# Optimization experiments

Hardware: AMD Instinct MI355X
Metric: run time of the kernel (lower is better)

Reference implementation:

```python
import jax, jax.numpy as jnp
import numpy as np

N_NODES = 50000
N_EDGES = 800000
DIM = 128
N_LAYERS = 3
OUT_DIM = 2
W_SCALE = 0.02


def setup_inputs() -> dict:
    key = jax.random.key(0)
    ks = jax.random.split(key, 12)
    x = jax.random.normal(ks[0], (N_NODES, DIM), dtype=jnp.float32)
    src = jax.random.randint(ks[1], (N_EDGES,), 0, N_NODES, dtype=jnp.int32)
    dst = jax.random.randint(ks[2], (N_EDGES,), 0, N_NODES, dtype=jnp.int32)
    Vw = jax.random.normal(ks[3], (N_LAYERS, DIM, DIM), dtype=jnp.float32) * W_SCALE
    Vb = jax.random.normal(ks[4], (N_LAYERS, DIM), dtype=jnp.float32) * W_SCALE
    Aw = jax.random.normal(ks[5], (N_LAYERS, DIM, DIM), dtype=jnp.float32) * W_SCALE
    Ab = jax.random.normal(ks[6], (N_LAYERS, DIM), dtype=jnp.float32) * W_SCALE
    Rw = jax.random.normal(ks[7], (N_LAYERS, DIM, DIM), dtype=jnp.float32) * W_SCALE
    Rb = jax.random.normal(ks[8], (N_LAYERS, DIM), dtype=jnp.float32) * W_SCALE
    out_w = jax.random.normal(ks[9], (OUT_DIM, DIM), dtype=jnp.float32) * W_SCALE
    out_b = jax.random.normal(ks[10], (OUT_DIM,), dtype=jnp.float32) * W_SCALE
    return {"x": x, "src": src, "dst": dst, "Vw": Vw, "Vb": Vb, "Aw": Aw,
            "Ab": Ab, "Rw": Rw, "Rb": Rb, "out_w": out_w, "out_b": out_b}


def reference(x, src, dst, Vw, Vb, Aw, Ab, Rw, Rb, out_w, out_b):
    # x: [N, d]; src/dst: [E] (edge (dst_i <- src_i): out[dst] += h[src], as torch.spmm(Adj, h))
    N = x.shape[0]
    h = x
    for l in range(Vw.shape[0]):
        # sum aggregation over neighbors; learn_eps=False adds self-loops -> + h
        agg = jax.ops.segment_sum(h[src], dst, num_segments=N) + h  # [N, d]
        ro = jnp.sum(h, axis=0, keepdims=True)                      # sum readout, [1, d]
        # trainable combine: relu(V(h) + A(agg) + R(readout)), R term broadcasts over nodes
        h = jax.nn.relu(h @ Vw[l].T + Vb[l]
                        + agg @ Aw[l].T + Ab[l]
                        + ro @ Rw[l].T + Rb[l])
    # node task, recursive_weighting=False: sigmoid(Linear(h))
    return jax.nn.sigmoid(h @ out_w.T + out_b)
```

## Files before the change

### kernel.cpp

```cpp
#include <hip/hip_runtime.h>
#include <cstdint>
#include <cstddef>

#define NN 50000
#define NE 800000
#define D 128
#define KK 256
#define NPAD 50048
#define GEMM_BLOCKS (NPAD / 64)
#define LDSW 136
#define BSTR 136
#define NBUCK 196
#define BCAP 5120
#define SCH 4096
#define SBLKS ((NE + SCH - 1) / SCH)
#define CVT_BLOCKS 391
#define PREP_BLOCKS 384
#define AGG_BLOCKS 12500

typedef __bf16 bf16x8 __attribute__((ext_vector_type(8)));
typedef float f32x4 __attribute__((ext_vector_type(4)));
typedef float f32x2 __attribute__((ext_vector_type(2)));
typedef unsigned short ushort;
typedef unsigned int uint;

__device__ __forceinline__ ushort f2b(float f) {
    uint u = __float_as_uint(f);
    uint r = (u + 0x7fffu + ((u >> 16) & 1u)) >> 16;
    return (ushort)r;
}
__device__ __forceinline__ float blo(uint u) { return __uint_as_float(u << 16); }
__device__ __forceinline__ float bhi(uint u) { return __uint_as_float(u & 0xffff0000u); }

__device__ __forceinline__ uint enc_n(float v) {
    int t = (int)(__float_as_uint(v) >> 22);
    int n = max(t - 252, min(t - 251, 1));
    return (uint)min(max(n, 0), 7);
}
__device__ __forceinline__ uint enc8(uint4 vv, float sf) {
    uint n0 = enc_n(blo(vv.x) * sf), n1 = enc_n(bhi(vv.x) * sf);
    uint n2 = enc_n(blo(vv.y) * sf), n3 = enc_n(bhi(vv.y) * sf);
    uint n4 = enc_n(blo(vv.z) * sf), n5 = enc_n(bhi(vv.z) * sf);
    uint n6 = enc_n(blo(vv.w) * sf), n7 = enc_n(bhi(vv.w) * sf);
    return n0 | (n1 << 4) | (n2 << 8) | (n3 << 12) |
           (n4 << 16) | (n5 << 20) | (n6 << 24) | (n7 << 28);
}
__device__ __forceinline__ void dec_acc(uint u, float* a) {
    uint lo = u & 0x0F0F0F0Fu;
    uint hi = (u >> 4) & 0x0F0F0F0Fu;
    uint b0 = __builtin_amdgcn_perm(0x4C484440u, 0x3C383000u, lo);
    uint b1 = __builtin_amdgcn_perm(0x4C484440u, 0x3C383000u, hi);
    f32x2 p;
    p = __builtin_amdgcn_cvt_pk_f32_fp8(b0, false); a[0] += p.x; a[2] += p.y;
    p = __builtin_amdgcn_cvt_pk_f32_fp8(b0, true);  a[4] += p.x; a[6] += p.y;
    p = __builtin_amdgcn_cvt_pk_f32_fp8(b1, false); a[1] += p.x; a[3] += p.y;
    p = __builtin_amdgcn_cvt_pk_f32_fp8(b1, true);  a[5] += p.x; a[7] += p.y;
}

__device__ __forceinline__ void red_col(const float* __restrict__ pblk, int nb,
                                        int j, float* __restrict__ dst,
                                        float* __restrict__ sred) {
    int t = threadIdx.x;
    float s = 0.f;
    for (int b = t; b < nb; b += 256) s += pblk[(size_t)b * D + j];
#pragma unroll
    for (int off = 32; off; off >>= 1) s += __shfl_xor(s, off);
    if ((t & 63) == 0) sred[t >> 6] = s;
    __syncthreads();
    if (t == 0) dst[j] = sred[0] + sred[1] + sred[2] + sred[3];
}

__global__ void k_zero(int* __restrict__ zone) { zone[threadIdx.x] = 0; }

__global__ void __launch_bounds__(256) k_build(
    const int* __restrict__ src, const int* __restrict__ dst,
    int* __restrict__ bfill, uint* __restrict__ packed,
    const float* __restrict__ x, ushort* __restrict__ hb,
    uint* __restrict__ hf4, float* __restrict__ pblk,
    const float* __restrict__ Vw, const float* __restrict__ Aw,
    ushort* __restrict__ W2) {
    __shared__ int cnt[256];
    __shared__ int base[256];
    __shared__ ushort pos[SCH];
    __shared__ float scol[D];
    int t = threadIdx.x;
    if (blockIdx.x < SBLKS) {
        int e0 = blockIdx.x * SCH, e1 = min(e0 + SCH, NE);
        cnt[t] = 0;
        __syncthreads();
        for (int e = e0 + t; e < e1; e += 256) {
            int b = dst[e] >> 8;
            pos[e - e0] = (ushort)atomicAdd(&cnt[b], 1);
        }
        __syncthreads();
        if (t < NBUCK && cnt[t])
            base[t] = atomicAdd(&bfill[t], cnt[t]) + t * BCAP;
        __syncthreads();
        for (int e = e0 + t; e < e1; e += 256) {
            int d = dst[e];
            int b = d >> 8;
            packed[base[b] + pos[e - e0]] = (uint)src[e] | ((uint)(d & 255) << 16);
        }
        return;
    }
    if (blockIdx.x < SBLKS + CVT_BLOCKS) {
        int bid = blockIdx.x - SBLKS;
        if (t < D) scol[t] = 0.f;
        __syncthreads();
        const float4* x4 = (const float4*)x;
        uint4* h8 = (uint4*)hb;
        float cs[8] = {0, 0, 0, 0, 0, 0, 0, 0};
        int bb = bid * 2048 + t;
#pragma unroll
        for (int i = 0; i < 8; i++) {
            int idx = bb + i * 256;
            if (idx < NN * D / 8) {
                float4 va = x4[idx * 2], vb = x4[idx * 2 + 1];
                cs[0] += va.x; cs[1] += va.y; cs[2] += va.z; cs[3] += va.w;
                cs[4] += vb.x; cs[5] += vb.y; cs[6] += vb.z; cs[7] += vb.w;
                uint4 o;
                o.x = (uint)f2b(va.x) | ((uint)f2b(va.y) << 16);
                o.y = (uint)f2b(va.z) | ((uint)f2b(va.w) << 16);
                o.z = (uint)f2b(vb.x) | ((uint)f2b(vb.y) << 16);
                o.w = (uint)f2b(vb.z) | ((uint)f2b(vb.w) << 16);
                h8[idx] = o;
                uint n0 = enc_n(fmaxf(va.x * 0.75f + 3.f, 0.f));
                uint n1 = enc_n(fmaxf(va.y * 0.75f + 3.f, 0.f));
                uint n2 = enc_n(fmaxf(va.z * 0.75f + 3.f, 0.f));
                uint n3 = enc_n(fmaxf(va.w * 0.75f + 3.f, 0.f));
                uint n4 = enc_n(fmaxf(vb.x * 0.75f + 3.f, 0.f));
                uint n5 = enc_n(fmaxf(vb.y * 0.75f + 3.f, 0.f));
                uint n6 = enc_n(fmaxf(vb.z * 0.75f + 3.f, 0.f));
                uint n7 = enc_n(fmaxf(vb.w * 0.75f + 3.f, 0.f));
                hf4[idx] = n0 | (n1 << 4) | (n2 << 8) | (n3 << 12) |
                           (n4 << 16) | (n5 << 20) | (n6 << 24) | (n7 << 28);
            }
        }
#pragma unroll
        for (int k = 0; k < 8; k++) {
            cs[k] += __shfl_xor(cs[k], 16);
            cs[k] += __shfl_xor(cs[k], 32);
        }
        if ((t & 63) < 16) {
            int c8 = (t & 15) * 8;
#pragma unroll
            for (int k = 0; k < 8; k++) atomicAdd(&scol[c8 + k], cs[k]);
        }
        __syncthreads();
        if (t < D) pblk[(size_t)bid * D + t] = scol[t];
        return;
    }
    int idx = (blockIdx.x - SBLKS - CVT_BLOCKS) * 256 + t;
    int k = idx & (KK - 1);
    int j = (idx >> 8) & (D - 1);
    int l = idx >> 15;
    float v = (k < D) ? Vw[((size_t)l * D + j) * D + k]
                      : Aw[((size_t)l * D + j) * D + (k - D)];
    W2[idx] = f2b(v);
}

__global__ void __launch_bounds__(512) k_bcsr(
    const uint* __restrict__ packed, const int* __restrict__ bfill,
    int* __restrict__ esrc, int2* __restrict__ rp2,
    const float* __restrict__ pblk, float* __restrict__ ro0) {
    __shared__ int hist[256];
    __shared__ int sc[256];
    __shared__ int start[256];
    __shared__ ushort pos[BCAP];
    __shared__ float sred[8];
    int t = threadIdx.x;
    if (blockIdx.x >= NBUCK) {
        int j = blockIdx.x - NBUCK;
        if (t < 256) {
            float s = 0.f;
            for (int b = t; b < CVT_BLOCKS; b += 256) s += pblk[(size_t)b * D + j];
#pragma unroll
            for (int off = 32; off; off >>= 1) s += __shfl_xor(s, off);
            if ((t & 63) == 0) sred[t >> 6] = s;
        }
        __syncthreads();
        if (t == 0) ro0[j] = sred[0] + sred[1] + sred[2] + sred[3];
        return;
    }
    int b = blockIdx.x;
    int lo = b * BCAP, cnt = bfill[b];
    if (t < 256) hist[t] = 0;
    __syncthreads();
    for (int i = t; i < cnt; i += 512) {
        int node = (packed[lo + i] >> 16) & 255;
        pos[i] = (ushort)atomicAdd(&hist[node], 1);
    }
    __syncthreads();
    int v = 0;
    if (t < 256) { v = hist[t]; sc[t] = v; }
    __syncthreads();
    for (int off = 1; off < 256; off <<= 1) {
        int u = 0;
        if (t < 256 && t >= off) u = sc[t - off];
        __syncthreads();
        if (t < 256) sc[t] += u;
        __syncthreads();
    }
    if (t < 256) {
        int excl = sc[t] - v;
        int node = b * 256 + t;
        if (node < NN) rp2[node] = make_int2(lo + excl, lo + excl + v);
        start[t] = lo + excl;
    }
    __syncthreads();
    for (int i = t; i < cnt; i += 512) {
        uint p = packed[lo + i];
        esrc[start[(p >> 16) & 255] + pos[i]] = (int)(p & 0xffffu);
    }
}

__global__ void __launch_bounds__(256) k_agg(
    const ushort* __restrict__ hb, const uint* __restrict__ hf4,
    const int2* __restrict__ rp2, const int* __restrict__ esrc,
    const float* __restrict__ slot, ushort* __restrict__ A1, int lay0,
    const float* __restrict__ pblk, float* __restrict__ ro_out) {
    if (blockIdx.x >= AGG_BLOCKS) {
        __shared__ float sred[8];
        int j = blockIdx.x - AGG_BLOCKS;
        red_col(pblk, GEMM_BLOCKS, j, ro_out, sred);
        return;
    }
    int wave = (blockIdx.x * blockDim.x + threadIdx.x) >> 6;
    int lane = threadIdx.x & 63;
    if (wave >= NN) return;
    int c = lane & 15, s = lane >> 4;
    float dsc = lay0 ? (4.f / 3.f) : fmaxf(slot[0], 0.5f) * (1.f / 3.f);
    float doff = lay0 ? 4.f : 0.f;
    float a[8] = {0, 0, 0, 0, 0, 0, 0, 0};
    int2 rp = rp2[wave];
    int e0 = rp.x, e1 = rp.y;
    int cnt = e1 - e0;
    int iters = (cnt + 3) >> 2;
    int i0 = e0 + s;
    for (int it = 0; it < iters; it += 4) {
        int ia = i0 + it * 4, ib = ia + 4, ic = ia + 8, id = ia + 12;
        uint ua = 0, ub = 0, uc = 0, ud = 0;
        if (ia < e1) ua = hf4[esrc[ia] * 16 + c];
        if (ib < e1) ub = hf4[esrc[ib] * 16 + c];
        if (ic < e1) uc = hf4[esrc[ic] * 16 + c];
        if (id < e1) ud = hf4[esrc[id] * 16 + c];
        dec_acc(ua, a);
        dec_acc(ub, a);
        dec_acc(uc, a);
        dec_acc(ud, a);
    }
#pragma unroll
    for (int k = 0; k < 8; k++) {
        a[k] += __shfl_xor(a[k], 16);
        a[k] += __shfl_xor(a[k], 32);
    }
    if (s == 0) {
        float cf = (float)cnt * doff;
        uint4 su = ((const uint4*)(hb + (size_t)wave * D))[c];
        float r0 = a[0] * dsc - cf + blo(su.x);
        float r1 = a[1] * dsc - cf + bhi(su.x);
        float r2 = a[2] * dsc - cf + blo(su.y);
        float r3 = a[3] * dsc - cf + bhi(su.y);
        float r4 = a[4] * dsc - cf + blo(su.z);
        float r5 = a[5] * dsc - cf + bhi(su.z);
        float r6 = a[6] * dsc - cf + blo(su.w);
        float r7 = a[7] * dsc - cf + bhi(su.w);
        uint4 o;
        o.x = (uint)f2b(r0) | ((uint)f2b(r1) << 16);
        o.y = (uint)f2b(r2) | ((uint)f2b(r3) << 16);
        o.z = (uint)f2b(r4) | ((uint)f2b(r5) << 16);
        o.w = (uint)f2b(r6) | ((uint)f2b(r7) << 16);
        ((uint4*)(A1 + (size_t)wave * D))[c] = o;
    }
}

template <bool LAST>
__global__ void __launch_bounds__(256, 4) k_gemm(
    const ushort* __restrict__ hbin, const ushort* __restrict__ A1,
    const ushort* __restrict__ W2, const float* __restrict__ ro,
    const float* __restrict__ Rw, const float* __restrict__ Vb,
    const float* __restrict__ Ab, const float* __restrict__ Rb,
    float* __restrict__ sclout,
    ushort* __restrict__ hout, uint* __restrict__ hf4out,
    float* __restrict__ pblk,
    const float* __restrict__ ow, const float* __restrict__ ob,
    float* __restrict__ outp) {
    __shared__ ushort lds[D * BSTR];
    __shared__ float scol[D];
    __shared__ float rbl[D];
    __shared__ float rosh[D];
    int t = threadIdx.x;
    int wave = t >> 6, lane = t & 63;
    int m = lane & 15, q = lane >> 4;
    int node0 = blockIdx.x * 64 + wave * 16;

    if (t < D) { rosh[t] = ro[t]; scol[t] = 0.f; }
    __syncthreads();

    {
        int j = t >> 1;
        const float4* rw4 = (const float4*)(Rw + (size_t)j * D + (t & 1) * 64);
        const float4* rr4 = (const float4*)(rosh + (t & 1) * 64);
        float s = 0.f;
#pragma unroll
        for (int k = 0; k < 16; k++) {
            float4 a = rw4[k], b = rr4[k];
            s += a.x * b.x + a.y * b.y + a.z * b.z + a.w * b.w;
        }
        s += __shfl_xor(s, 1);
        if ((t & 1) == 0) rbl[j] = s + Vb[j] + Ab[j] + Rb[j];
    }

    bf16x8 selff[4], aggf[4];
    {
        const ushort* ap = hbin + (size_t)(node0 + m) * D + q * 8;
        const ushort* gp = A1 + (size_t)(node0 + m) * D + q * 8;
#pragma unroll
        for (int j = 0; j < 4; j++) {
            selff[j] = *(const bf16x8*)(ap + j * 32);
            aggf[j] = *(const bf16x8*)(gp + j * 32);
        }
    }

    f32x4 acc[8];
#pragma unroll
    for (int j = 0; j < 8; j++) acc[j] = (f32x4){0.f, 0.f, 0.f, 0.f};
    const ushort* bl = lds + m * BSTR + q * 8;

    {
        const uint4* ws = (const uint4*)W2;
#pragma unroll
        for (int i = 0; i < 8; i++) {
            int idx = t + i * 256;
            int row = idx >> 4;
            int cu = idx & 15;
            *(uint4*)(lds + row * BSTR + cu * 8) = ws[row * 32 + cu];
        }
    }
    __syncthreads();
#pragma unroll
    for (int kt = 0; kt < 4; kt++) {
        bf16x8 a = selff[kt];
#pragma unroll
        for (int j = 0; j < 8; j++) {
            bf16x8 b = *(const bf16x8*)(bl + j * 16 * BSTR + kt * 32);
            acc[j] = __builtin_amdgcn_mfma_f32_16x16x32_bf16(a, b, acc[j], 0, 0, 0);
        }
    }
    __syncthreads();

    {
        const uint4* ws = (const uint4*)W2;
#pragma unroll
        for (int i = 0; i < 8; i++) {
            int idx = t + i * 256;
            int row = idx >> 4;
            int cu = idx & 15;
            *(uint4*)(lds + row * BSTR + cu * 8) = ws[row * 32 + 16 + cu];
        }
    }
    __syncthreads();
#pragma unroll
    for (int kt = 0; kt < 4; kt++) {
        bf16x8 a = aggf[kt];
#pragma unroll
        for (int j = 0; j < 8; j++) {
            bf16x8 b = *(const bf16x8*)(bl + j * 16 * BSTR + kt * 32);
            acc[j] = __builtin_amdgcn_mfma_f32_16x16x32_bf16(a, b, acc[j], 0, 0, 0);
        }
    }
    __syncthreads();

    float rb[8];
#pragma unroll
    for (int j = 0; j < 8; j++) rb[j] = rbl[j * 16 + m];
    ushort* mytile = lds + wave * 16 * LDSW;
    float psum[8] = {0, 0, 0, 0, 0, 0, 0, 0};
#pragma unroll
    for (int j = 0; j < 8; j++) {
        f32x4 v = acc[j];
#pragma unroll
        for (int r = 0; r < 4; r++) {
            int row = q * 4 + r;
            float val = fmaxf(v[r] + rb[j], 0.f);
            if (!LAST) { if (node0 + row < NN) psum[j] += val; }
            mytile[row * LDSW + j * 16 + m] = f2b(val);
        }
    }

    if (!LAST) {
        float mx = fmaxf(fabsf(rbl[lane]), fabsf(rbl[lane + 64]));
#pragma unroll
        for (int off = 32; off; off >>= 1) mx = fmaxf(mx, __shfl_xor(mx, off));
        float sf = 3.f / fmaxf(mx, 0.5f);
        if (t == 0) sclout[0] = mx;
#pragma unroll
        for (int j = 0; j < 8; j++) atomicAdd(&scol[j * 16 + m], psum[j]);
        __syncthreads();
#pragma unroll
        for (int it = 0; it < 4; it++) {
            int row = it * 4 + q;
            int grow = node0 + row;
            if (grow < NN) {
                uint4 vv = *(const uint4*)(mytile + row * LDSW + m * 8);
                *(uint4*)(hout + (size_t)grow * D + m * 8) = vv;
                hf4out[(size_t)grow * 16 + m] = enc8(vv, sf);
            }
        }
        if (t < D) pblk[(size_t)blockIdx.x * D + t] = scol[t];
    } else {
        __syncthreads();
        float2 a0 = ((const float2*)ow)[lane];
        float2 a1 = ((const float2*)(ow + D))[lane];
        float b0 = ob[0], b1 = ob[1];
        for (int r = 0; r < 16; r++) {
            int node = node0 + r;
            uint u = ((const uint*)(mytile + r * LDSW))[lane];
            float vx = blo(u), vy = bhi(u);
            float p0 = vx * a0.x + vy * a0.y;
            float p1 = vx * a1.x + vy * a1.y;
#pragma unroll
            for (int off = 32; off; off >>= 1) {
                p0 += __shfl_xor(p0, off);
                p1 += __shfl_xor(p1, off);
            }
            if (lane == 0 && node < NN) {
                outp[(size_t)node * 2 + 0] = 1.f / (1.f + expf(-(p0 + b0)));
                outp[(size_t)node * 2 + 1] = 1.f / (1.f + expf(-(p1 + b1)));
            }
        }
    }
}

extern "C" void kernel_launch(void* const* d_in, const int* in_sizes, int n_in,
                              void* d_out, int out_size, void* d_ws, size_t ws_size,
                              hipStream_t stream) {
    const float* x   = (const float*)d_in[0];
    const int*   src = (const int*)d_in[1];
    const int*   dst = (const int*)d_in[2];
    const float* Vw  = (const float*)d_in[3];
    const float* Vb  = (const float*)d_in[4];
    const float* Aw  = (const float*)d_in[5];
    const float* Ab  = (const float*)d_in[6];
    const float* Rw  = (const float*)d_in[7];
    const float* Rb  = (const float*)d_in[8];
    const float* ow  = (const float*)d_in[9];
    const float* ob  = (const float*)d_in[10];
    float* out = (float*)d_out;

    char* w = (char*)d_ws;
    ushort* hb0    = (ushort*)w; w += (size_t)NPAD * D * 2;
    ushort* hb1    = (ushort*)w; w += (size_t)NPAD * D * 2;
    ushort* A1     = (ushort*)w; w += (size_t)NPAD * D * 2;
    uint*   hf4a   = (uint*)w;   w += (size_t)NN * 16 * 4;
    uint*   hf4b   = (uint*)w;   w += (size_t)NN * 16 * 4;
    ushort* W2     = (ushort*)w; w += (size_t)3 * D * KK * 2;
    int*    zone   = (int*)w;    w += (size_t)1024 * 4;
    float*  ro     = (float*)zone;
    float*  scl    = (float*)(zone + 512);
    int*    bfill  = zone + 520;
    uint*   packed = (uint*)w;   w += (size_t)NBUCK * BCAP * 4;
    int*    esrc   = (int*)w;    w += (size_t)NBUCK * BCAP * 4;
    int2*   rp2    = (int2*)w;   w += (size_t)NN * 8;
    float*  pblk   = (float*)w;  w += (size_t)GEMM_BLOCKS * D * 4;

    k_zero<<<1, 1024, 0, stream>>>(zone);
    k_build<<<SBLKS + CVT_BLOCKS + PREP_BLOCKS, 256, 0, stream>>>(
        src, dst, bfill, packed, x, hb0, hf4a, pblk, Vw, Aw, W2);
    k_bcsr<<<NBUCK + D, 512, 0, stream>>>(packed, bfill, esrc, rp2, pblk, ro);

    const ushort* hin = hb0;
    const uint* f4in = hf4a;
    ushort* hbufs[2] = {hb1, hb0};
    uint* f4bufs[2] = {hf4b, hf4a};
    for (int l = 0; l < 3; l++) {
        int agrid = AGG_BLOCKS + (l > 0 ? D : 0);
        k_agg<<<agrid, 256, 0, stream>>>(hin, f4in, rp2, esrc, scl + l, A1,
                                         l == 0 ? 1 : 0, pblk,
                                         (float*)(ro + (size_t)l * D));
        ushort* hnext = hbufs[l & 1];
        uint* f4next = f4bufs[l & 1];
        if (l < 2) {
            k_gemm<false><<<GEMM_BLOCKS, 256, 0, stream>>>(
                hin, A1, W2 + (size_t)l * D * KK, ro + (size_t)l * D,
                Rw + (size_t)l * D * D, Vb + (size_t)l * D, Ab + (size_t)l * D,
                Rb + (size_t)l * D, scl + l + 1, hnext, f4next, pblk,
                nullptr, nullptr, nullptr);
        } else {
            k_gemm<true><<<GEMM_BLOCKS, 256, 0, stream>>>(
                hin, A1, W2 + (size_t)l * D * KK, ro + (size_t)l * D,
                Rw + (size_t)l * D * D, Vb + (size_t)l * D, Ab + (size_t)l * D,
                Rb + (size_t)l * D, nullptr, nullptr, nullptr, nullptr,
                ow, ob, out);
        }
        hin = hnext;
        f4in = f4next;
    }
}
```

Before: 285.7 us.

## Regroup setup kernels: run CSR build alongside conversion, defer layer-0 readout

The edge scatter now runs in its own kernel. The per-bucket CSR construction is merged with the x-to-bf16/fp4 conversion and weight packing into a single 512-thread kernel, so those independent jobs share one launch instead of waiting behind each other. The layer-0 column-sum reduction moves into the first aggregation launch, and the zeroing kernel becomes a hipMemsetAsync. The aim is to cut launch count and serial gaps in setup. The cost is a larger block size for the conversion work, which may change occupancy.

```diff
diff --git a/kernel.cpp b/kernel.cpp
--- a/kernel.cpp
+++ b/kernel.cpp
@@ -15,7 +15,7 @@
 #define SCH 4096
 #define SBLKS ((NE + SCH - 1) / SCH)
 #define CVT_BLOCKS 391
-#define PREP_BLOCKS 384
+#define PREP_BLOCKS 192
 #define AGG_BLOCKS 12500
 
 typedef __bf16 bf16x8 __attribute__((ext_vector_type(8)));
@@ -57,54 +57,79 @@
     p = __builtin_amdgcn_cvt_pk_f32_fp8(b1, true);  a[5] += p.x; a[7] += p.y;
 }
 
-__device__ __forceinline__ void red_col(const float* __restrict__ pblk, int nb,
-                                        int j, float* __restrict__ dst,
-                                        float* __restrict__ sred) {
+__global__ void __launch_bounds__(256) k_scat(
+    const int* __restrict__ src, const int* __restrict__ dst,
+    int* __restrict__ bfill, uint* __restrict__ packed) {
+    __shared__ int cnt[256];
+    __shared__ int base[256];
+    __shared__ ushort pos[SCH];
     int t = threadIdx.x;
-    float s = 0.f;
-    for (int b = t; b < nb; b += 256) s += pblk[(size_t)b * D + j];
-#pragma unroll
-    for (int off = 32; off; off >>= 1) s += __shfl_xor(s, off);
-    if ((t & 63) == 0) sred[t >> 6] = s;
-    __syncthreads();
-    if (t == 0) dst[j] = sred[0] + sred[1] + sred[2] + sred[3];
-}
-
-__global__ void k_zero(int* __restrict__ zone) { zone[threadIdx.x] = 0; }
-
-__global__ void __launch_bounds__(256) k_build(
-    const int* __restrict__ src, const int* __restrict__ dst,
-    int* __restrict__ bfill, uint* __restrict__ packed,
+    int e0 = blockIdx.x * SCH, e1 = min(e0 + SCH, NE);
+    cnt[t] = 0;
+    __syncthreads();
+    for (int e = e0 + t; e < e1; e += 256) {
+        int b = dst[e] >> 8;
+        pos[e - e0] = (ushort)atomicAdd(&cnt[b], 1);
+    }
+    __syncthreads();
+    if (t < NBUCK && cnt[t])
+        base[t] = atomicAdd(&bfill[t], cnt[t]) + t * BCAP;
+    __syncthreads();
+    for (int e = e0 + t; e < e1; e += 256) {
+        int d = dst[e];
+        int b = d >> 8;
+        packed[base[b] + pos[e - e0]] = (uint)src[e] | ((uint)(d & 255) << 16);
+    }
+}
+
+__global__ void __launch_bounds__(512) k_rest(
+    const uint* __restrict__ packed, const int* __restrict__ bfill,
+    int* __restrict__ esrc, int2* __restrict__ rp2,
     const float* __restrict__ x, ushort* __restrict__ hb,
     uint* __restrict__ hf4, float* __restrict__ pblk,
     const float* __restrict__ Vw, const float* __restrict__ Aw,
     ushort* __restrict__ W2) {
-    __shared__ int cnt[256];
-    __shared__ int base[256];
-    __shared__ ushort pos[SCH];
+    __shared__ int hist[256];
+    __shared__ int sc[256];
+    __shared__ int start[256];
+    __shared__ ushort pos[BCAP];
     __shared__ float scol[D];
     int t = threadIdx.x;
-    if (blockIdx.x < SBLKS) {
-        int e0 = blockIdx.x * SCH, e1 = min(e0 + SCH, NE);
-        cnt[t] = 0;
-        __syncthreads();
-        for (int e = e0 + t; e < e1; e += 256) {
-            int b = dst[e] >> 8;
-            pos[e - e0] = (ushort)atomicAdd(&cnt[b], 1);
-        }
-        __syncthreads();
-        if (t < NBUCK && cnt[t])
-            base[t] = atomicAdd(&bfill[t], cnt[t]) + t * BCAP;
-        __syncthreads();
-        for (int e = e0 + t; e < e1; e += 256) {
-            int d = dst[e];
-            int b = d >> 8;
-            packed[base[b] + pos[e - e0]] = (uint)src[e] | ((uint)(d & 255) << 16);
+    if (blockIdx.x < NBUCK) {
+        int b = blockIdx.x;
+        int lo = b * BCAP, cnt = bfill[b];
+        if (t < 256) hist[t] = 0;
+        __syncthreads();
+        for (int i = t; i < cnt; i += 512) {
+            int node = (packed[lo + i] >> 16) & 255;
+            pos[i] = (ushort)atomicAdd(&hist[node], 1);
+        }
+        __syncthreads();
+        int v = 0;
+        if (t < 256) { v = hist[t]; sc[t] = v; }
+        __syncthreads();
+        for (int off = 1; off < 256; off <<= 1) {
+            int u = 0;
+            if (t < 256 && t >= off) u = sc[t - off];
+            __syncthreads();
+            if (t < 256) sc[t] += u;
+            __syncthreads();
+        }
+        if (t < 256) {
+            int excl = sc[t] - v;
+            int node = b * 256 + t;
+            if (node < NN) rp2[node] = make_int2(lo + excl, lo + excl + v);
+            start[t] = lo + excl;
+        }
+        __syncthreads();
+        for (int i = t; i < cnt; i += 512) {
+            uint p = packed[lo + i];
+            esrc[start[(p >> 16) & 255] + pos[i]] = (int)(p & 0xffffu);
         }
         return;
     }
-    if (blockIdx.x < SBLKS + CVT_BLOCKS) {
-        int bid = blockIdx.x - SBLKS;
+    if (blockIdx.x < NBUCK + CVT_BLOCKS) {
+        int bid = blockIdx.x - NBUCK;
         if (t < D) scol[t] = 0.f;
         __syncthreads();
         const float4* x4 = (const float4*)x;
@@ -112,8 +137,8 @@
         float cs[8] = {0, 0, 0, 0, 0, 0, 0, 0};
         int bb = bid * 2048 + t;
 #pragma unroll
-        for (int i = 0; i < 8; i++) {
-            int idx = bb + i * 256;
+        for (int i = 0; i < 4; i++) {
+            int idx = bb + i * 512;
             if (idx < NN * D / 8) {
                 float4 va = x4[idx * 2], vb = x4[idx * 2 + 1];
                 cs[0] += va.x; cs[1] += va.y; cs[2] += va.z; cs[3] += va.w;
@@ -150,7 +175,7 @@
         if (t < D) pblk[(size_t)bid * D + t] = scol[t];
         return;
     }
-    int idx = (blockIdx.x - SBLKS - CVT_BLOCKS) * 256 + t;
+    int idx = (blockIdx.x - NBUCK - CVT_BLOCKS) * 512 + t;
     int k = idx & (KK - 1);
     int j = (idx >> 8) & (D - 1);
     int l = idx >> 15;
@@ -159,70 +184,22 @@
     W2[idx] = f2b(v);
 }
 
-__global__ void __launch_bounds__(512) k_bcsr(
-    const uint* __restrict__ packed, const int* __restrict__ bfill,
-    int* __restrict__ esrc, int2* __restrict__ rp2,
-    const float* __restrict__ pblk, float* __restrict__ ro0) {
-    __shared__ int hist[256];
-    __shared__ int sc[256];
-    __shared__ int start[256];
-    __shared__ ushort pos[BCAP];
-    __shared__ float sred[8];
-    int t = threadIdx.x;
-    if (blockIdx.x >= NBUCK) {
-        int j = blockIdx.x - NBUCK;
-        if (t < 256) {
-            float s = 0.f;
-            for (int b = t; b < CVT_BLOCKS; b += 256) s += pblk[(size_t)b * D + j];
-#pragma unroll
-            for (int off = 32; off; off >>= 1) s += __shfl_xor(s, off);
-            if ((t & 63) == 0) sred[t >> 6] = s;
-        }
-        __syncthreads();
-        if (t == 0) ro0[j] = sred[0] + sred[1] + sred[2] + sred[3];
-        return;
-    }
-    int b = blockIdx.x;
-    int lo = b * BCAP, cnt = bfill[b];
-    if (t < 256) hist[t] = 0;
-    __syncthreads();
-    for (int i = t; i < cnt; i += 512) {
-        int node = (packed[lo + i] >> 16) & 255;
-        pos[i] = (ushort)atomicAdd(&hist[node], 1);
-    }
-    __syncthreads();
-    int v = 0;
-    if (t < 256) { v = hist[t]; sc[t] = v; }
-    __syncthreads();
-    for (int off = 1; off < 256; off <<= 1) {
-        int u = 0;
-        if (t < 256 && t >= off) u = sc[t - off];
-        __syncthreads();
-        if (t < 256) sc[t] += u;
-        __syncthreads();
-    }
-    if (t < 256) {
-        int excl = sc[t] - v;
-        int node = b * 256 + t;
-        if (node < NN) rp2[node] = make_int2(lo + excl, lo + excl + v);
-        start[t] = lo + excl;
-    }
-    __syncthreads();
-    for (int i = t; i < cnt; i += 512) {
-        uint p = packed[lo + i];
-        esrc[start[(p >> 16) & 255] + pos[i]] = (int)(p & 0xffffu);
-    }
-}
-
 __global__ void __launch_bounds__(256) k_agg(
     const ushort* __restrict__ hb, const uint* __restrict__ hf4,
     const int2* __restrict__ rp2, const int* __restrict__ esrc,
     const float* __restrict__ slot, ushort* __restrict__ A1, int lay0,
-    const float* __restrict__ pblk, float* __restrict__ ro_out) {
+    const float* __restrict__ pblk, int nred, float* __restrict__ ro_out) {
     if (blockIdx.x >= AGG_BLOCKS) {
         __shared__ float sred[8];
         int j = blockIdx.x - AGG_BLOCKS;
-        red_col(pblk, GEMM_BLOCKS, j, ro_out, sred);
+        int t = threadIdx.x;
+        float s = 0.f;
+        for (int b = t; b < nred; b += 256) s += pblk[(size_t)b * D + j];
+#pragma unroll
+        for (int off = 32; off; off >>= 1) s += __shfl_xor(s, off);
+        if ((t & 63) == 0) sred[t >> 6] = s;
+        __syncthreads();
+        if (t == 0) ro_out[j] = sred[0] + sred[1] + sred[2] + sred[3];
         return;
     }
     int wave = (blockIdx.x * blockDim.x + threadIdx.x) >> 6;
@@ -464,20 +441,19 @@
     int2*   rp2    = (int2*)w;   w += (size_t)NN * 8;
     float*  pblk   = (float*)w;  w += (size_t)GEMM_BLOCKS * D * 4;
 
-    k_zero<<<1, 1024, 0, stream>>>(zone);
-    k_build<<<SBLKS + CVT_BLOCKS + PREP_BLOCKS, 256, 0, stream>>>(
-        src, dst, bfill, packed, x, hb0, hf4a, pblk, Vw, Aw, W2);
-    k_bcsr<<<NBUCK + D, 512, 0, stream>>>(packed, bfill, esrc, rp2, pblk, ro);
+    hipMemsetAsync(zone, 0, 1024 * 4, stream);
+    k_scat<<<SBLKS, 256, 0, stream>>>(src, dst, bfill, packed);
+    k_rest<<<NBUCK + CVT_BLOCKS + PREP_BLOCKS, 512, 0, stream>>>(
+        packed, bfill, esrc, rp2, x, hb0, hf4a, pblk, Vw, Aw, W2);
 
     const ushort* hin = hb0;
     const uint* f4in = hf4a;
     ushort* hbufs[2] = {hb1, hb0};
     uint* f4bufs[2] = {hf4b, hf4a};
     for (int l = 0; l < 3; l++) {
-        int agrid = AGG_BLOCKS + (l > 0 ? D : 0);
-        k_agg<<<agrid, 256, 0, stream>>>(hin, f4in, rp2, esrc, scl + l, A1,
-                                         l == 0 ? 1 : 0, pblk,
-                                         (float*)(ro + (size_t)l * D));
+        k_agg<<<AGG_BLOCKS + D, 256, 0, stream>>>(
+            hin, f4in, rp2, esrc, scl + l, A1, l == 0 ? 1 : 0, pblk,
+            l == 0 ? CVT_BLOCKS : GEMM_BLOCKS, (float*)(ro + (size_t)l * D));
         ushort* hnext = hbufs[l & 1];
         uint* f4next = f4bufs[l & 1];
         if (l < 2) {
```

Measured after the change: 289.6 us. Within noise of the previous version (+1.3%).
